# Performance work log

Hardware: AMD Instinct MI355X
Metric: run time of the kernel (lower is better)

The kernel has to match this reference:

```python
import jax, jax.numpy as jnp
import numpy as np

V, E, H, L, B = 32004, 512, 512, 128, 64  # vocab(+4), emb, hidden, seq_len, batch


def setup_inputs() -> dict:
    key = jax.random.key(0)
    ks = jax.random.split(key, 8)
    emb = jax.random.normal(ks[0], (V, E), jnp.float32) * 0.02
    emb = emb.at[0].set(0.0)  # padding_idx = PAD = 0
    Wx_f = jax.random.normal(ks[1], (E, 3 * H), jnp.float32) * 0.05
    Wh_f = jax.random.normal(ks[2], (H, 3 * H), jnp.float32) * 0.05
    b_f = jnp.zeros((3 * H,), jnp.float32)
    Wx_b = jax.random.normal(ks[3], (E, 3 * H), jnp.float32) * 0.05
    Wh_b = jax.random.normal(ks[4], (H, 3 * H), jnp.float32) * 0.05
    b_b = jnp.zeros((3 * H,), jnp.float32)
    xs = jax.random.randint(ks[5], (L, B), 0, V)
    xs_mask = jnp.ones((L, B), jnp.float32)
    return {"xs": xs, "xs_mask": xs_mask, "emb": emb,
            "Wx_f": Wx_f, "Wh_f": Wh_f, "b_f": b_f,
            "Wx_b": Wx_b, "Wh_b": Wh_b, "b_b": b_b}


def _gru_scan(xs_e, mask, Wx, Wh, b, reverse):
    # Precompute all input-to-gate projections in one big GEMM: [L,B,3H]
    xw = jnp.einsum('lbe,eg->lbg', xs_e, Wx) + b

    def step(h, inp):
        xw_t, m = inp                       # [B,3H], [B]
        hw = h @ Wh                         # [B,3H]
        xz, xr, xh = jnp.split(xw_t, 3, -1)
        hz, hr, hh = jnp.split(hw, 3, -1)
        z = jax.nn.sigmoid(xz + hz)
        r = jax.nn.sigmoid(xr + hr)
        h_tilde = jnp.tanh(xh + r * hh)
        h_new = (1.0 - z) * h + z * h_tilde
        m = m[:, None]
        h_new = m * h_new + (1.0 - m) * h   # masked timesteps keep previous state
        return h_new, h_new

    h0 = jnp.zeros((xs_e.shape[1], Wh.shape[0]), xs_e.dtype)
    _, hs = jax.lax.scan(step, h0, (xw, mask), reverse=reverse)
    return hs  # [L,B,H], time-ordered (reverse=True already yields original order)


def reference(xs, xs_mask, emb, Wx_f, Wh_f, b_f, Wx_b, Wh_b, b_b):
    xs_e = emb[xs]                                   # [L,B,E]
    right = _gru_scan(xs_e, xs_mask, Wx_f, Wh_f, b_f, reverse=False)
    left = _gru_scan(xs_e, xs_mask, Wx_b, Wh_b, b_b, reverse=True)
    r1 = jnp.concatenate([right, left], axis=-1)      # [L,B,2H]
    r2 = left[0]                                      # final backward state (after t=0)
    return r1, r2
```

## Files before the change

kernel.cpp:

```cpp
#include <hip/hip_runtime.h>
#include <stdint.h>

typedef _Float16 f16;
typedef _Float16 f16x8 __attribute__((ext_vector_type(8)));
typedef float    f32x4 __attribute__((ext_vector_type(4)));
typedef unsigned long long u64;

#define L_    128
#define B_    64
#define E_    512
#define H_    512
#define G3    1536
#define NCOL  3072

__device__ __forceinline__ float sigm_(float x){ return 1.0f/(1.0f + __expf(-x)); }
__device__ __forceinline__ float tanh_(float x){ return 1.0f - 2.0f/(__expf(2.0f*x) + 1.0f); }

__global__ __launch_bounds__(256) void k_zero(uint4* flags){
  flags[(size_t)blockIdx.x*256 + threadIdx.x] = make_uint4(0,0,0,0);
}

__global__ __launch_bounds__(256) void k_embed(const int* __restrict__ xs,
                                               const float* __restrict__ emb,
                                               f16* __restrict__ Xe){
  int row = blockIdx.x*2 + (threadIdx.x >> 7);
  int c   = (threadIdx.x & 127) * 4;
  int idx = xs[row];
  float4 v = *(const float4*)(emb + (size_t)idx*E_ + c);
  union { f16 h[4]; uint2 u; } p;
  p.h[0] = (f16)v.x; p.h[1] = (f16)v.y; p.h[2] = (f16)v.z; p.h[3] = (f16)v.w;
  *(uint2*)(Xe + (size_t)row*E_ + c) = p.u;
}

__global__ __launch_bounds__(256) void k_transpose(const float* __restrict__ Wx_f, const float* __restrict__ Wx_b,
                                                   const float* __restrict__ Wh_f, const float* __restrict__ Wh_b,
                                                   f16* __restrict__ WxT, f16* __restrict__ WhT){
  int mat = blockIdx.z;
  const float* src = mat==0 ? Wx_f : mat==1 ? Wx_b : mat==2 ? Wh_f : Wh_b;
  f16* dst = (mat < 2) ? (WxT + (size_t)mat*G3*E_) : (WhT + (size_t)(mat-2)*G3*H_);
  int n0 = blockIdx.x*64, k0 = blockIdx.y*64;
  __shared__ f16 tile[64][65];
  int tid = threadIdx.x;
  for (int i=0;i<16;i++){
    int r = i*4 + (tid>>6);
    int c = tid & 63;
    tile[r][c] = (f16)src[(size_t)(k0+r)*G3 + n0 + c];
  }
  __syncthreads();
  for (int i=0;i<16;i++){
    int n = i*4 + (tid>>6);
    int k = tid & 63;
    dst[(size_t)(n0+n)*512 + k0 + k] = tile[k][n];
  }
}

__global__ __launch_bounds__(256) void k_gemm(const f16* __restrict__ Xe, const f16* __restrict__ WxT,
                                              const float* __restrict__ bf, const float* __restrict__ bb,
                                              f16* __restrict__ xw2){
  __shared__ __align__(16) f16 sA[128*32];
  __shared__ __align__(16) f16 sB[128*32];
  const int tid = threadIdx.x;
  const int l = tid & 63, w = tid >> 6;
  const int wr = w >> 1, wc = w & 1;
  const int m0 = blockIdx.y*128, n0 = blockIdx.x*128;
  const int rl = l & 15, sg = l >> 4;
  f32x4 acc[4][4] = {};
  for (int kk=0; kk<16; ++kk){
    __syncthreads();
    for (int i=0;i<2;i++){
      int c = i*256 + tid; int row = c>>2, s = c&3;
      int sw = s ^ ((row>>1)&3);
      *(uint4*)&sA[row*32 + sw*8] = *(const uint4*)(Xe  + (size_t)(m0+row)*512 + kk*32 + s*8);
      *(uint4*)&sB[row*32 + sw*8] = *(const uint4*)(WxT + (size_t)(n0+row)*512 + kk*32 + s*8);
    }
    __syncthreads();
    f16x8 a[4], b[4];
    for (int mi=0;mi<4;mi++){ int m=(wr*4+mi)*16+rl; a[mi] = *(const f16x8*)&sA[m*32 + ((sg^((m>>1)&3))*8)]; }
    for (int nj=0;nj<4;nj++){ int n=(wc*4+nj)*16+rl; b[nj] = *(const f16x8*)&sB[n*32 + ((sg^((n>>1)&3))*8)]; }
    for (int mi=0;mi<4;mi++)
      for (int nj=0;nj<4;nj++)
        acc[mi][nj] = __builtin_amdgcn_mfma_f32_16x16x32_f16(a[mi], b[nj], acc[mi][nj], 0,0,0);
  }
  for (int nj=0;nj<4;nj++){
    int n = n0 + (wc*4+nj)*16 + rl;
    float bias = (n < G3) ? bf[n] : bb[n-G3];
    for (int mi=0;mi<4;mi++){
      int sub = (wr*4+mi)*16 + sg*4;
      int t   = (m0 + sub) >> 6;
      int b0  = sub & 63;
      union { f16 h[4]; uint2 u; } p;
      for (int r=0;r<4;r++) p.h[r] = (f16)(acc[mi][nj][r] + bias);
      *(uint2*)(xw2 + ((size_t)t*NCOL + n)*B_ + b0) = p.u;
    }
  }
}

__global__ __launch_bounds__(256) void k_scan(const f16* __restrict__ xw2, const f16* __restrict__ WhT,
                                              f16* __restrict__ hbuf, const float* __restrict__ mask,
                                              float* __restrict__ out, unsigned* __restrict__ flags){
  const int dir = blockIdx.x >> 5, g = blockIdx.x & 31;
  __shared__ __align__(16) f16 sW[48*512];
  __shared__ __align__(16) f16 sOut[64*16];
  const int tid = threadIdx.x, l = tid & 63, wv = tid >> 6;
  {
    const f16* base = WhT + (size_t)dir*G3*512;
    int cs = tid & 15;
    for (int r = tid>>4; r < 48; r += 16){
      int rowg = (r>>4)*512 + g*16 + (r&15);
      const uint4* src = (const uint4*)(base + (size_t)rowg*512);
      for (int j=0;j<4;j++){
        int s = cs*4 + j;
        *(uint4*)&sW[r*512 + ((s^(r&7))*8)] = src[s];
      }
    }
  }
  float hstate[4] = {0.f,0.f,0.f,0.f};
  const int fl   = l & 15;
  const int sg   = l >> 4;
  const int mb   = wv*16 + sg*4;
  const int arow = wv*16 + fl;
  const int swzB = fl & 7;
  float* out2 = out + (size_t)L_*B_*1024;
  const unsigned* myflags = flags + dir*32*32;
  const int pb = tid >> 2, pf = (tid & 3)*4;

  __syncthreads();
  for (int ti=0; ti<128; ++ti){
    const int t = dir ? (127 - ti) : ti;
    size_t xb = ((size_t)t*NCOL + dir*G3 + g*16 + fl)*B_ + mb;
    union { uint2 u; f16 h[4]; } xzv, xrv, xhv;
    xzv.u = *(const uint2*)(xw2 + xb);
    xrv.u = *(const uint2*)(xw2 + xb + (size_t)512*B_);
    xhv.u = *(const uint2*)(xw2 + xb + (size_t)1024*B_);
    float4 mv4 = *(const float4*)(mask + t*B_ + mb);
    f32x4 az = {0,0,0,0}, arr = {0,0,0,0}, ah = {0,0,0,0};
    if (ti){
      unsigned tgt = (unsigned)ti;
      const unsigned* fp = myflags + (l & 31)*32;
      while (true){
        unsigned f = __hip_atomic_load(fp, __ATOMIC_RELAXED, __HIP_MEMORY_SCOPE_AGENT);
        if (__all((int)(f >= tgt))) break;
        __builtin_amdgcn_s_sleep(1);
      }
      const u64* hq = (const u64*)(hbuf + ((size_t)dir*2 + (ti&1))*(64*512)) + (size_t)arow*128;
      u64 q[32];
      #pragma unroll
      for (int kk=0;kk<16;kk++){
        int j = (kk*4 + sg)*2;
        q[2*kk  ] = __hip_atomic_load(hq + j,     __ATOMIC_RELAXED, __HIP_MEMORY_SCOPE_AGENT);
        q[2*kk+1] = __hip_atomic_load(hq + j + 1, __ATOMIC_RELAXED, __HIP_MEMORY_SCOPE_AGENT);
      }
      #pragma unroll
      for (int kk=0;kk<16;kk++){
        int s = kk*4 + sg;
        union { u64 d[2]; f16x8 h; } a;
        a.d[0] = q[2*kk]; a.d[1] = q[2*kk+1];
        f16x8 b0 = *(const f16x8*)&sW[(     fl)*512 + ((s^swzB)*8)];
        f16x8 b1 = *(const f16x8*)&sW[(16 + fl)*512 + ((s^swzB)*8)];
        f16x8 b2 = *(const f16x8*)&sW[(32 + fl)*512 + ((s^swzB)*8)];
        az  = __builtin_amdgcn_mfma_f32_16x16x32_f16(a.h, b0, az , 0,0,0);
        arr = __builtin_amdgcn_mfma_f32_16x16x32_f16(a.h, b1, arr, 0,0,0);
        ah  = __builtin_amdgcn_mfma_f32_16x16x32_f16(a.h, b2, ah , 0,0,0);
      }
    }
    #pragma unroll
    for (int r=0;r<4;r++){
      float z  = sigm_((float)xzv.h[r] + az[r]);
      float rr = sigm_((float)xrv.h[r] + arr[r]);
      float ht = tanh_((float)xhv.h[r] + rr*ah[r]);
      float mv = (&mv4.x)[r];
      float hn = (1.0f - z)*hstate[r] + z*ht;
      hn = mv*hn + (1.0f - mv)*hstate[r];
      hstate[r] = hn;
    }
    if (ti < 127){
      #pragma unroll
      for (int r=0;r<4;r++) sOut[(mb + r)*16 + fl] = (f16)hstate[r];
      __syncthreads();
      {
        f16* hb = hbuf + ((size_t)dir*2 + ((ti&1)^1))*(64*512);
        u64 v = *(const u64*)&sOut[pb*16 + pf];
        __hip_atomic_store((u64*)(hb + (size_t)pb*512 + g*16 + pf), v,
                           __ATOMIC_RELAXED, __HIP_MEMORY_SCOPE_AGENT);
      }
      __syncthreads();
      if (tid == 0)
        __hip_atomic_store(flags + (dir*32 + g)*32, (unsigned)(ti+1),
                           __ATOMIC_RELAXED, __HIP_MEMORY_SCOPE_AGENT);
    }
    #pragma unroll
    for (int r=0;r<4;r++){
      int m = mb + r;
      out[((size_t)(t*B_+m))*1024 + dir*512 + g*16 + fl] = hstate[r];
    }
    if (dir==1 && t==0){
      #pragma unroll
      for (int r=0;r<4;r++)
        out2[(size_t)(mb+r)*512 + g*16 + fl] = hstate[r];
    }
  }
}

extern "C" void kernel_launch(void* const* d_in, const int* in_sizes, int n_in,
                              void* d_out, int out_size, void* d_ws, size_t ws_size,
                              hipStream_t stream){
  const int*   xs      = (const int*)  d_in[0];
  const float* xs_mask = (const float*)d_in[1];
  const float* emb     = (const float*)d_in[2];
  const float* Wx_f    = (const float*)d_in[3];
  const float* Wh_f    = (const float*)d_in[4];
  const float* b_f     = (const float*)d_in[5];
  const float* Wx_b    = (const float*)d_in[6];
  const float* Wh_b    = (const float*)d_in[7];
  const float* b_b     = (const float*)d_in[8];

  char* w = (char*)d_ws;
  f16*      Xe    = (f16*)(w);
  f16*      WxT   = (f16*)(w + 8388608);
  f16*      WhT   = (f16*)(w + 11534336);
  f16*      xw2   = (f16*)(w + 14680064);
  f16*      hbuf  = (f16*)(w + 65011712);
  unsigned* flags = (unsigned*)(w + 65273856);
  float*    out   = (float*)d_out;

  k_zero     <<<dim3(2),       dim3(256), 0, stream>>>((uint4*)flags);
  k_embed    <<<dim3(4096),    dim3(256), 0, stream>>>(xs, emb, Xe);
  k_transpose<<<dim3(24,8,4),  dim3(256), 0, stream>>>(Wx_f, Wx_b, Wh_f, Wh_b, WxT, WhT);
  k_gemm     <<<dim3(24,64),   dim3(256), 0, stream>>>(Xe, WxT, b_f, b_b, xw2);
  k_scan     <<<dim3(64),      dim3(256), 0, stream>>>(xw2, WhT, hbuf, xs_mask, out, flags);
}
```

Baseline: 731.4 us.

## Swap MFMA operands in GRU scan, per-wave flags, register-cached weights

The recurrent scan now computes the transposed product (weights as A, hidden state as B), so each lane owns four consecutive hidden units of one batch row. That lets it write its f16 state straight to global memory without the shared-memory staging and the two block-wide barriers per step. Synchronisation moves to per-wave flags, and half the Wh slice is preloaded into registers to cut LDS reads on the critical path. The GEMM output layout changes to row-major [t*B+b, NCOL], and output stores become float4. The trade-off is much higher register pressure (launch_bounds 256,1) and a more fragile flag protocol that depends on s_waitcnt ordering.

```diff
diff --git a/kernel.cpp b/kernel.cpp
--- a/kernel.cpp
+++ b/kernel.cpp
@@ -56,7 +56,7 @@
 
 __global__ __launch_bounds__(256) void k_gemm(const f16* __restrict__ Xe, const f16* __restrict__ WxT,
                                               const float* __restrict__ bf, const float* __restrict__ bb,
-                                              f16* __restrict__ xw2){
+                                              f16* __restrict__ xw){
   __shared__ __align__(16) f16 sA[128*32];
   __shared__ __align__(16) f16 sB[128*32];
   const int tid = threadIdx.x;
@@ -85,22 +85,18 @@
     int n = n0 + (wc*4+nj)*16 + rl;
     float bias = (n < G3) ? bf[n] : bb[n-G3];
     for (int mi=0;mi<4;mi++){
-      int sub = (wr*4+mi)*16 + sg*4;
-      int t   = (m0 + sub) >> 6;
-      int b0  = sub & 63;
-      union { f16 h[4]; uint2 u; } p;
-      for (int r=0;r<4;r++) p.h[r] = (f16)(acc[mi][nj][r] + bias);
-      *(uint2*)(xw2 + ((size_t)t*NCOL + n)*B_ + b0) = p.u;
-    }
-  }
-}
-
-__global__ __launch_bounds__(256) void k_scan(const f16* __restrict__ xw2, const f16* __restrict__ WhT,
-                                              f16* __restrict__ hbuf, const float* __restrict__ mask,
-                                              float* __restrict__ out, unsigned* __restrict__ flags){
+      int mrow = m0 + (wr*4+mi)*16 + sg*4;
+      for (int r=0;r<4;r++)
+        xw[(size_t)(mrow+r)*NCOL + n] = (f16)(acc[mi][nj][r] + bias);
+    }
+  }
+}
+
+__global__ __launch_bounds__(256, 1) void k_scan(const f16* __restrict__ xw, const f16* __restrict__ WhT,
+                                                 f16* __restrict__ hbuf, const float* __restrict__ mask,
+                                                 float* __restrict__ out, unsigned* __restrict__ flags){
   const int dir = blockIdx.x >> 5, g = blockIdx.x & 31;
   __shared__ __align__(16) f16 sW[48*512];
-  __shared__ __align__(16) f16 sOut[64*16];
   const int tid = threadIdx.x, l = tid & 63, wv = tid >> 6;
   {
     const f16* base = WhT + (size_t)dir*G3*512;
@@ -114,89 +110,94 @@
       }
     }
   }
+  const int fl = l & 15, sg = l >> 4;
+  const int b  = wv*16 + fl;
+  const int swz = fl & 7;
+  __syncthreads();
+  f16x8 paz[8], par[8], pah[8];
+  #pragma unroll
+  for (int kk=0;kk<8;kk++){
+    int s = kk*4 + sg;
+    paz[kk] = *(const f16x8*)&sW[(     fl)*512 + ((s^swz)*8)];
+    par[kk] = *(const f16x8*)&sW[(16 + fl)*512 + ((s^swz)*8)];
+    pah[kk] = *(const f16x8*)&sW[(32 + fl)*512 + ((s^swz)*8)];
+  }
   float hstate[4] = {0.f,0.f,0.f,0.f};
-  const int fl   = l & 15;
-  const int sg   = l >> 4;
-  const int mb   = wv*16 + sg*4;
-  const int arow = wv*16 + fl;
-  const int swzB = fl & 7;
   float* out2 = out + (size_t)L_*B_*1024;
-  const unsigned* myflags = flags + dir*32*32;
-  const int pb = tid >> 2, pf = (tid & 3)*4;
-
-  __syncthreads();
+  unsigned* myflag = flags + (size_t)(dir*32 + g)*32 + wv*8;
+  const unsigned* pollp = flags + (size_t)dir*32*32 + (size_t)(l&31)*32 + wv*8;
+
   for (int ti=0; ti<128; ++ti){
     const int t = dir ? (127 - ti) : ti;
-    size_t xb = ((size_t)t*NCOL + dir*G3 + g*16 + fl)*B_ + mb;
+    size_t xr = (size_t)(t*B_ + b)*NCOL + (size_t)dir*G3 + g*16 + sg*4;
     union { uint2 u; f16 h[4]; } xzv, xrv, xhv;
-    xzv.u = *(const uint2*)(xw2 + xb);
-    xrv.u = *(const uint2*)(xw2 + xb + (size_t)512*B_);
-    xhv.u = *(const uint2*)(xw2 + xb + (size_t)1024*B_);
-    float4 mv4 = *(const float4*)(mask + t*B_ + mb);
-    f32x4 az = {0,0,0,0}, arr = {0,0,0,0}, ah = {0,0,0,0};
+    xzv.u = *(const uint2*)(xw + xr);
+    xrv.u = *(const uint2*)(xw + xr + 512);
+    xhv.u = *(const uint2*)(xw + xr + 1024);
+    float mv = mask[t*B_ + b];
+    f32x4 az = {0,0,0,0}, ar = {0,0,0,0}, ah = {0,0,0,0};
     if (ti){
       unsigned tgt = (unsigned)ti;
-      const unsigned* fp = myflags + (l & 31)*32;
       while (true){
-        unsigned f = __hip_atomic_load(fp, __ATOMIC_RELAXED, __HIP_MEMORY_SCOPE_AGENT);
+        unsigned f = __hip_atomic_load(pollp, __ATOMIC_RELAXED, __HIP_MEMORY_SCOPE_AGENT);
         if (__all((int)(f >= tgt))) break;
         __builtin_amdgcn_s_sleep(1);
       }
-      const u64* hq = (const u64*)(hbuf + ((size_t)dir*2 + (ti&1))*(64*512)) + (size_t)arow*128;
+      const u64* hq = (const u64*)(hbuf + ((size_t)dir*2 + (ti&1))*(64*512)) + (size_t)b*128;
       u64 q[32];
       #pragma unroll
       for (int kk=0;kk<16;kk++){
-        int j = (kk*4 + sg)*2;
+        int j = kk*8 + sg*2;
         q[2*kk  ] = __hip_atomic_load(hq + j,     __ATOMIC_RELAXED, __HIP_MEMORY_SCOPE_AGENT);
         q[2*kk+1] = __hip_atomic_load(hq + j + 1, __ATOMIC_RELAXED, __HIP_MEMORY_SCOPE_AGENT);
       }
       #pragma unroll
-      for (int kk=0;kk<16;kk++){
+      for (int kk=0;kk<8;kk++){
+        union { u64 d[2]; f16x8 h; } bf;
+        bf.d[0] = q[2*kk]; bf.d[1] = q[2*kk+1];
+        az = __builtin_amdgcn_mfma_f32_16x16x32_f16(paz[kk], bf.h, az, 0,0,0);
+        ar = __builtin_amdgcn_mfma_f32_16x16x32_f16(par[kk], bf.h, ar, 0,0,0);
+        ah = __builtin_amdgcn_mfma_f32_16x16x32_f16(pah[kk], bf.h, ah, 0,0,0);
+      }
+      #pragma unroll
+      for (int kk=8;kk<16;kk++){
         int s = kk*4 + sg;
-        union { u64 d[2]; f16x8 h; } a;
-        a.d[0] = q[2*kk]; a.d[1] = q[2*kk+1];
-        f16x8 b0 = *(const f16x8*)&sW[(     fl)*512 + ((s^swzB)*8)];
-        f16x8 b1 = *(const f16x8*)&sW[(16 + fl)*512 + ((s^swzB)*8)];
-        f16x8 b2 = *(const f16x8*)&sW[(32 + fl)*512 + ((s^swzB)*8)];
-        az  = __builtin_amdgcn_mfma_f32_16x16x32_f16(a.h, b0, az , 0,0,0);
-        arr = __builtin_amdgcn_mfma_f32_16x16x32_f16(a.h, b1, arr, 0,0,0);
-        ah  = __builtin_amdgcn_mfma_f32_16x16x32_f16(a.h, b2, ah , 0,0,0);
+        union { u64 d[2]; f16x8 h; } bf;
+        bf.d[0] = q[2*kk]; bf.d[1] = q[2*kk+1];
+        f16x8 a0 = *(const f16x8*)&sW[(     fl)*512 + ((s^swz)*8)];
+        f16x8 a1 = *(const f16x8*)&sW[(16 + fl)*512 + ((s^swz)*8)];
+        f16x8 a2 = *(const f16x8*)&sW[(32 + fl)*512 + ((s^swz)*8)];
+        az = __builtin_amdgcn_mfma_f32_16x16x32_f16(a0, bf.h, az, 0,0,0);
+        ar = __builtin_amdgcn_mfma_f32_16x16x32_f16(a1, bf.h, ar, 0,0,0);
+        ah = __builtin_amdgcn_mfma_f32_16x16x32_f16(a2, bf.h, ah, 0,0,0);
       }
     }
     #pragma unroll
     for (int r=0;r<4;r++){
       float z  = sigm_((float)xzv.h[r] + az[r]);
-      float rr = sigm_((float)xrv.h[r] + arr[r]);
+      float rr = sigm_((float)xrv.h[r] + ar[r]);
       float ht = tanh_((float)xhv.h[r] + rr*ah[r]);
-      float mv = (&mv4.x)[r];
       float hn = (1.0f - z)*hstate[r] + z*ht;
       hn = mv*hn + (1.0f - mv)*hstate[r];
       hstate[r] = hn;
     }
     if (ti < 127){
-      #pragma unroll
-      for (int r=0;r<4;r++) sOut[(mb + r)*16 + fl] = (f16)hstate[r];
-      __syncthreads();
-      {
-        f16* hb = hbuf + ((size_t)dir*2 + ((ti&1)^1))*(64*512);
-        u64 v = *(const u64*)&sOut[pb*16 + pf];
-        __hip_atomic_store((u64*)(hb + (size_t)pb*512 + g*16 + pf), v,
+      union { f16 h[4]; u64 u; } pk;
+      #pragma unroll
+      for (int r=0;r<4;r++) pk.h[r] = (f16)hstate[r];
+      f16* hb = hbuf + ((size_t)dir*2 + ((ti&1)^1))*(64*512);
+      __hip_atomic_store((u64*)(hb + (size_t)b*512 + g*16 + sg*4), pk.u,
+                         __ATOMIC_RELAXED, __HIP_MEMORY_SCOPE_AGENT);
+      asm volatile("s_waitcnt vmcnt(0)" ::: "memory");
+      if (l == 0)
+        __hip_atomic_store(myflag, (unsigned)(ti+1),
                            __ATOMIC_RELAXED, __HIP_MEMORY_SCOPE_AGENT);
-      }
-      __syncthreads();
-      if (tid == 0)
-        __hip_atomic_store(flags + (dir*32 + g)*32, (unsigned)(ti+1),
-                           __ATOMIC_RELAXED, __HIP_MEMORY_SCOPE_AGENT);
-    }
-    #pragma unroll
-    for (int r=0;r<4;r++){
-      int m = mb + r;
-      out[((size_t)(t*B_+m))*1024 + dir*512 + g*16 + fl] = hstate[r];
-    }
-    if (dir==1 && t==0){
-      #pragma unroll
-      for (int r=0;r<4;r++)
-        out2[(size_t)(mb+r)*512 + g*16 + fl] = hstate[r];
+    }
+    {
+      float4 v = make_float4(hstate[0], hstate[1], hstate[2], hstate[3]);
+      *(float4*)(out + ((size_t)(t*B_ + b))*1024 + dir*512 + g*16 + sg*4) = v;
+      if (dir==1 && t==0)
+        *(float4*)(out2 + (size_t)b*512 + g*16 + sg*4) = v;
     }
   }
 }
@@ -218,7 +219,7 @@
   f16*      Xe    = (f16*)(w);
   f16*      WxT   = (f16*)(w + 8388608);
   f16*      WhT   = (f16*)(w + 11534336);
-  f16*      xw2   = (f16*)(w + 14680064);
+  f16*      xw    = (f16*)(w + 14680064);
   f16*      hbuf  = (f16*)(w + 65011712);
   unsigned* flags = (unsigned*)(w + 65273856);
   float*    out   = (float*)d_out;
@@ -226,6 +227,6 @@
   k_zero     <<<dim3(2),       dim3(256), 0, stream>>>((uint4*)flags);
   k_embed    <<<dim3(4096),    dim3(256), 0, stream>>>(xs, emb, Xe);
   k_transpose<<<dim3(24,8,4),  dim3(256), 0, stream>>>(Wx_f, Wx_b, Wh_f, Wh_b, WxT, WhT);
-  k_gemm     <<<dim3(24,64),   dim3(256), 0, stream>>>(Xe, WxT, b_f, b_b, xw2);
-  k_scan     <<<dim3(64),      dim3(256), 0, stream>>>(xw2, WhT, hbuf, xs_mask, out, flags);
-}
+  k_gemm     <<<dim3(24,64),   dim3(256), 0, stream>>>(Xe, WxT, b_f, b_b, xw);
+  k_scan     <<<dim3(64),      dim3(256), 0, stream>>>(xw, WhT, hbuf, xs_mask, out, flags);
+}
```

Result: slower. 851.4 us (+16.4%).

## Keep recurrent weights in registers and use per-wave flags instead of block barriers

Applied to the files above, without the earlier changes.

The scan kernel now loads its slice of the recurrent weight matrix from LDS into registers once, before the time loop, so the MFMA inner loop no longer reads LDS every step. The LDS staging buffer and the two __syncthreads per step are removed. Each wave writes its hidden-state values directly as 16-bit atomic stores and raises its own flag after a vmcnt wait, and consumer waves poll only the flag of the matching producer wave. This cuts barrier and LDS latency on the serial recurrence critical path, at the cost of heavy register pressure (48 f16x8 values held per lane) and many small scattered stores in place of coalesced 8-byte ones.

```diff
diff --git a/kernel.cpp b/kernel.cpp
--- a/kernel.cpp
+++ b/kernel.cpp
@@ -95,12 +95,11 @@
   }
 }
 
-__global__ __launch_bounds__(256) void k_scan(const f16* __restrict__ xw2, const f16* __restrict__ WhT,
-                                              f16* __restrict__ hbuf, const float* __restrict__ mask,
-                                              float* __restrict__ out, unsigned* __restrict__ flags){
+__global__ __launch_bounds__(256, 1) void k_scan(const f16* __restrict__ xw2, const f16* __restrict__ WhT,
+                                                 f16* __restrict__ hbuf, const float* __restrict__ mask,
+                                                 float* __restrict__ out, unsigned* __restrict__ flags){
   const int dir = blockIdx.x >> 5, g = blockIdx.x & 31;
   __shared__ __align__(16) f16 sW[48*512];
-  __shared__ __align__(16) f16 sOut[64*16];
   const int tid = threadIdx.x, l = tid & 63, wv = tid >> 6;
   {
     const f16* base = WhT + (size_t)dir*G3*512;
@@ -114,17 +113,30 @@
       }
     }
   }
-  float hstate[4] = {0.f,0.f,0.f,0.f};
-  const int fl   = l & 15;
-  const int sg   = l >> 4;
+  const int fl = l & 15, sg = l >> 4;
   const int mb   = wv*16 + sg*4;
   const int arow = wv*16 + fl;
-  const int swzB = fl & 7;
+  const int swz  = fl & 7;
+  __syncthreads();
+  f16x8 pz[16], pr[16], ph[16];
+  #pragma unroll
+  for (int kk=0;kk<16;kk++){
+    int s = kk*4 + sg;
+    pz[kk] = *(const f16x8*)&sW[(     fl)*512 + ((s^swz)*8)];
+    pr[kk] = *(const f16x8*)&sW[(16 + fl)*512 + ((s^swz)*8)];
+    ph[kk] = *(const f16x8*)&sW[(32 + fl)*512 + ((s^swz)*8)];
+  }
+  #pragma unroll
+  for (int kk=0;kk<16;kk++){
+    asm volatile("" : "+v"(pz[kk]));
+    asm volatile("" : "+v"(pr[kk]));
+    asm volatile("" : "+v"(ph[kk]));
+  }
+  float hstate[4] = {0.f,0.f,0.f,0.f};
   float* out2 = out + (size_t)L_*B_*1024;
-  const unsigned* myflags = flags + dir*32*32;
-  const int pb = tid >> 2, pf = (tid & 3)*4;
-
-  __syncthreads();
+  unsigned* myflag = flags + (size_t)(dir*32 + g)*32 + wv*8;
+  const unsigned* pollp = flags + (size_t)dir*1024 + (size_t)(l&31)*32 + wv*8;
+
   for (int ti=0; ti<128; ++ti){
     const int t = dir ? (127 - ti) : ti;
     size_t xb = ((size_t)t*NCOL + dir*G3 + g*16 + fl)*B_ + mb;
@@ -133,12 +145,11 @@
     xrv.u = *(const uint2*)(xw2 + xb + (size_t)512*B_);
     xhv.u = *(const uint2*)(xw2 + xb + (size_t)1024*B_);
     float4 mv4 = *(const float4*)(mask + t*B_ + mb);
-    f32x4 az = {0,0,0,0}, arr = {0,0,0,0}, ah = {0,0,0,0};
+    f32x4 az = {0,0,0,0}, ar = {0,0,0,0}, ah = {0,0,0,0};
     if (ti){
       unsigned tgt = (unsigned)ti;
-      const unsigned* fp = myflags + (l & 31)*32;
       while (true){
-        unsigned f = __hip_atomic_load(fp, __ATOMIC_RELAXED, __HIP_MEMORY_SCOPE_AGENT);
+        unsigned f = __hip_atomic_load(pollp, __ATOMIC_RELAXED, __HIP_MEMORY_SCOPE_AGENT);
         if (__all((int)(f >= tgt))) break;
         __builtin_amdgcn_s_sleep(1);
       }
@@ -146,27 +157,23 @@
       u64 q[32];
       #pragma unroll
       for (int kk=0;kk<16;kk++){
-        int j = (kk*4 + sg)*2;
+        int j = kk*8 + sg*2;
         q[2*kk  ] = __hip_atomic_load(hq + j,     __ATOMIC_RELAXED, __HIP_MEMORY_SCOPE_AGENT);
         q[2*kk+1] = __hip_atomic_load(hq + j + 1, __ATOMIC_RELAXED, __HIP_MEMORY_SCOPE_AGENT);
       }
       #pragma unroll
       for (int kk=0;kk<16;kk++){
-        int s = kk*4 + sg;
         union { u64 d[2]; f16x8 h; } a;
         a.d[0] = q[2*kk]; a.d[1] = q[2*kk+1];
-        f16x8 b0 = *(const f16x8*)&sW[(     fl)*512 + ((s^swzB)*8)];
-        f16x8 b1 = *(const f16x8*)&sW[(16 + fl)*512 + ((s^swzB)*8)];
-        f16x8 b2 = *(const f16x8*)&sW[(32 + fl)*512 + ((s^swzB)*8)];
-        az  = __builtin_amdgcn_mfma_f32_16x16x32_f16(a.h, b0, az , 0,0,0);
-        arr = __builtin_amdgcn_mfma_f32_16x16x32_f16(a.h, b1, arr, 0,0,0);
-        ah  = __builtin_amdgcn_mfma_f32_16x16x32_f16(a.h, b2, ah , 0,0,0);
+        az = __builtin_amdgcn_mfma_f32_16x16x32_f16(a.h, pz[kk], az, 0,0,0);
+        ar = __builtin_amdgcn_mfma_f32_16x16x32_f16(a.h, pr[kk], ar, 0,0,0);
+        ah = __builtin_amdgcn_mfma_f32_16x16x32_f16(a.h, ph[kk], ah, 0,0,0);
       }
     }
     #pragma unroll
     for (int r=0;r<4;r++){
       float z  = sigm_((float)xzv.h[r] + az[r]);
-      float rr = sigm_((float)xrv.h[r] + arr[r]);
+      float rr = sigm_((float)xrv.h[r] + ar[r]);
       float ht = tanh_((float)xhv.h[r] + rr*ah[r]);
       float mv = (&mv4.x)[r];
       float hn = (1.0f - z)*hstate[r] + z*ht;
@@ -174,18 +181,16 @@
       hstate[r] = hn;
     }
     if (ti < 127){
-      #pragma unroll
-      for (int r=0;r<4;r++) sOut[(mb + r)*16 + fl] = (f16)hstate[r];
-      __syncthreads();
-      {
-        f16* hb = hbuf + ((size_t)dir*2 + ((ti&1)^1))*(64*512);
-        u64 v = *(const u64*)&sOut[pb*16 + pf];
-        __hip_atomic_store((u64*)(hb + (size_t)pb*512 + g*16 + pf), v,
+      f16* hb = hbuf + ((size_t)dir*2 + ((ti&1)^1))*(64*512);
+      #pragma unroll
+      for (int r=0;r<4;r++){
+        union { f16 h; unsigned short u; } pk; pk.h = (f16)hstate[r];
+        __hip_atomic_store((unsigned short*)(hb + (size_t)(mb+r)*512 + g*16 + fl), pk.u,
                            __ATOMIC_RELAXED, __HIP_MEMORY_SCOPE_AGENT);
       }
-      __syncthreads();
-      if (tid == 0)
-        __hip_atomic_store(flags + (dir*32 + g)*32, (unsigned)(ti+1),
+      asm volatile("s_waitcnt vmcnt(0)" ::: "memory");
+      if (l == 0)
+        __hip_atomic_store(myflag, (unsigned)(ti+1),
                            __ATOMIC_RELAXED, __HIP_MEMORY_SCOPE_AGENT);
     }
     #pragma unroll
```

New measurement: 866.1 us. 18.4% more time.
